# Kernel optimization log

Measured on AMD Instinct MI355X. Metric: run time of the kernel, lower is better.

The kernel has to match this reference:

```python
import jax, jax.numpy as jnp
import numpy as np

N = 8192       # num_nodes
F_IN = 128     # num_features
H = 32         # hidden_dim
C = 10         # num_classes
E = 262144     # num_edges (avg degree 32)
EPS = 1e-5     # BatchNorm1d eps


def setup_inputs() -> dict:
    key = jax.random.key(0)
    ks = jax.random.split(key, 24)
    rn = lambda k, shape, s=0.05: jax.random.normal(k, shape, jnp.float32) * s
    z = lambda n: jnp.zeros((n,), jnp.float32)
    return {
        "b": jax.random.normal(ks[0], (N, N), jnp.float32),
        "x": jax.random.normal(ks[1], (N, F_IN), jnp.float32),
        "edge_index": jax.random.randint(ks[2], (2, E), 0, N, jnp.int32),
        # GCNConv weights (stored [in,out]) + biases
        "W0": rn(ks[3], (F_IN, H)), "bc0": z(H),
        "W1": rn(ks[4], (H, H)),    "bc1": z(H),
        # BatchNorm affine params
        "g0": jnp.ones((H,), jnp.float32), "be0": z(H),
        "g1": jnp.ones((H,), jnp.float32), "be1": z(H),
        # autoencoder Linears (stored [in,out])
        "Wa0": rn(ks[5], (N, H)), "ba0": z(H),
        "Wa1": rn(ks[6], (H, H)), "ba1": z(H),
        "Wa2": rn(ks[7], (H, H)), "ba2": z(H),
        "Wa3": rn(ks[8], (H, N)), "ba3": z(N),
        # jump classifier: Linear(num_layers*H, C)
        "Wj": rn(ks[9], (2 * H, C)), "bj": z(C),
    }


def _gcn_conv(x, W, bias, src, dst):
    # PyG GCNConv: D^{-1/2}(A+I)D^{-1/2} X W + bias (src/dst already include self-loops)
    h = x @ W                                             # [N, out]
    deg = jax.ops.segment_sum(jnp.ones(src.shape[0], h.dtype), dst, num_segments=N)
    dinv = jax.lax.rsqrt(deg)                             # deg >= 1 due to self-loops
    norm = dinv[src] * dinv[dst]                          # [E+N]
    agg = jax.ops.segment_sum(norm[:, None] * h[src], dst, num_segments=N)
    return agg + bias


def _bn(x, g, b):
    # BatchNorm1d in training mode: batch stats over node dim, biased variance
    m = jnp.mean(x, axis=0)
    v = jnp.var(x, axis=0)
    return g * (x - m) * jax.lax.rsqrt(v + EPS) + b


def reference(b, x, edge_index, W0, bc0, W1, bc1, g0, be0, g1, be1,
              Wa0, ba0, Wa1, ba1, Wa2, ba2, Wa3, ba3, Wj, bj):
    loop = jnp.arange(N, dtype=edge_index.dtype)
    src = jnp.concatenate([edge_index[0], loop])
    dst = jnp.concatenate([edge_index[1], loop])

    # layer 0
    h = jax.nn.relu(_bn(_gcn_conv(x, W0, bc0, src, dst), g0, be0))
    x0 = h
    b = b @ Wa0 + ba0          # [N, H]
    h = h + b
    # layer 1
    h = jax.nn.relu(_bn(_gcn_conv(h, W1, bc1, src, dst), g1, be1))
    x1 = h
    b = b @ Wa1 + ba1
    # (torch computes x = x1 + b here, but it is dead after the last layer)
    # decoder tail: autoencoder[2], autoencoder[3]
    b = b @ Wa2 + ba2
    b = b @ Wa3 + ba3          # [N, N]

    out = jnp.concatenate([x0, x1], axis=1) @ Wj + bj
    return jax.nn.log_softmax(out, axis=-1), b
```

## Files before the change

### kernel.cpp

```cpp
#include <hip/hip_runtime.h>
#include <math.h>

#define NN 8192
#define FIN 128
#define HD 32
#define NC 10
#define NE 262144
#define EPSBN 1e-5f

typedef short short8 __attribute__((ext_vector_type(8)));
typedef float f32x4 __attribute__((ext_vector_type(4)));

__device__ __forceinline__ float bf2f(unsigned short b) {
  unsigned int u = ((unsigned int)b) << 16;
  float f;
  __builtin_memcpy(&f, &u, 4);
  return f;
}
__device__ __forceinline__ unsigned short f2bf(float f) {
  unsigned int u;
  __builtin_memcpy(&u, &f, 4);
  u = u + 0x7fffu + ((u >> 16) & 1u);
  return (unsigned short)(u >> 16);
}
__device__ __forceinline__ short8 ld_bf8(const unsigned short* p) {
  uint4 u = *(const uint4*)p;
  return __builtin_bit_cast(short8, u);
}
__device__ __forceinline__ float ldin(const void* p, int i, int isf) {
  if (isf) return ((const float*)p)[i];
  return bf2f(((const unsigned short*)p)[i]);
}

__global__ void detect_k(const void* __restrict__ b, int* __restrict__ flag) {
  const unsigned short* p = (const unsigned short*)b;
  int t = threadIdx.x;
  unsigned short s = p[2 * t];
  int e = (s >> 7) & 0xFF;
  int hit = (e >= 110 && e <= 135) ? 1 : 0;
  __shared__ int cnt[256];
  cnt[t] = hit;
  __syncthreads();
  for (int o = 128; o > 0; o >>= 1) {
    if (t < o) cnt[t] += cnt[t + o];
    __syncthreads();
  }
  if (t == 0) flag[0] = (cnt[0] < 128) ? 1 : 0;
}

__global__ void prep_T(const void* __restrict__ Wa1, const void* __restrict__ ba1,
                       const void* __restrict__ Wa2, const void* __restrict__ ba2,
                       const int* __restrict__ flg, float* __restrict__ T, float* __restrict__ vv) {
  int isf = *flg;
  __shared__ float sW1[1024], sW2[1024];
  int t = threadIdx.x;
  sW1[t] = ldin(Wa1, t, isf);
  sW2[t] = ldin(Wa2, t, isf);
  __syncthreads();
  {
    int c = t >> 5, c2 = t & 31;
    float acc = 0.f;
    for (int k = 0; k < 32; k++) acc += sW1[c * 32 + k] * sW2[k * 32 + c2];
    T[c * 32 + c2] = acc;
  }
  if (t < 32) {
    float acc = ldin(ba2, t, isf);
    for (int k = 0; k < 32; k++) acc += ldin(ba1, k, isf) * sW2[k * 32 + t];
    vv[t] = acc;
  }
}

__global__ void compute_Rp(const void* __restrict__ Wa3, const void* __restrict__ ba3,
                           const float* __restrict__ T, const float* __restrict__ vv,
                           const int* __restrict__ flg,
                           float* __restrict__ r2, unsigned short* __restrict__ Rp) {
  int isf = *flg;
  __shared__ float sT[1024], sv[32];
  int t = threadIdx.x;
  for (int i = t; i < 1024; i += 256) sT[i] = T[i];
  if (t < 32) sv[t] = vv[t];
  __syncthreads();
  int j = blockIdx.x * 256 + t;
  float w3[32];
  for (int c = 0; c < 32; c++) w3[c] = ldin(Wa3, c * NN + j, isf);
  float rr = ldin(ba3, j, isf);
  for (int c = 0; c < 32; c++) rr += sv[c] * w3[c];
  r2[j] = rr;
  float Rcol[32];
  for (int c = 0; c < 32; c++) {
    float acc = 0.f;
    for (int cp = 0; cp < 32; cp++) acc += sT[c * 32 + cp] * w3[cp];
    Rcol[c] = acc;
  }
  int jt = j >> 4, n = j & 15;
  for (int q = 0; q < 4; q++)
    for (int jj = 0; jj < 8; jj++)
      Rp[(size_t)(jt * 64 + q * 16 + n) * 8 + jj] = f2bf(Rcol[q * 8 + jj]);
}

__global__ void pack_Bp(const void* __restrict__ Wa0, const int* __restrict__ flg,
                        unsigned short* __restrict__ Bp) {
  int isf = *flg;
  int tid = blockIdx.x * 256 + threadIdx.x;
  int kb = tid >> 7;
  int h = (tid >> 6) & 1;
  int L = tid & 63;
  int q = L >> 4, n = L & 15;
  int base_k = kb * 32 + q * 8;
  if (isf) {
    const float* W = (const float*)Wa0;
    for (int j = 0; j < 8; j++)
      Bp[(size_t)((kb * 2 + h) * 64 + L) * 8 + j] = f2bf(W[(base_k + j) * HD + h * 16 + n]);
  } else {
    const unsigned short* W = (const unsigned short*)Wa0;
    for (int j = 0; j < 8; j++)
      Bp[(size_t)((kb * 2 + h) * 64 + L) * 8 + j] = W[(base_k + j) * HD + h * 16 + n];
  }
}

__global__ void deg_k(const int* __restrict__ dst, int* __restrict__ deg) {
  int e = blockIdx.x * 256 + threadIdx.x;
  atomicAdd(&deg[dst[e]], 1);
}

__global__ void csr_scan(const int* __restrict__ deg, int* __restrict__ rowp,
                         float* __restrict__ dinvf) {
  __shared__ int ps[1024];
  int t = threadIdx.x;
  int base = t * 8;
  int loc[8];
  int s = 0;
  for (int j = 0; j < 8; j++) {
    int d = deg[base + j];
    loc[j] = s;
    s += d;
    dinvf[base + j] = rsqrtf((float)d + 1.0f);
  }
  ps[t] = s;
  __syncthreads();
  for (int off = 1; off < 1024; off <<= 1) {
    int v = (t >= off) ? ps[t - off] : 0;
    __syncthreads();
    if (t >= off) ps[t] += v;
    __syncthreads();
  }
  int ex = (t > 0) ? ps[t - 1] : 0;
  for (int j = 0; j < 8; j++) rowp[base + j] = ex + loc[j];
  if (t == 1023) rowp[NN] = ex + s;
}

__global__ void csr_fill(const int* __restrict__ src, const int* __restrict__ dst,
                         const int* __restrict__ rowp, int* __restrict__ cnt,
                         int* __restrict__ col) {
  int e = blockIdx.x * 256 + threadIdx.x;
  int d = dst[e];
  int pos = atomicAdd(&cnt[d], 1);
  col[rowp[d] + pos] = src[e];
}

__global__ void gemm_x_w0(const void* __restrict__ x, const void* __restrict__ W0,
                          const float* __restrict__ dinvf, const int* __restrict__ flg,
                          float* __restrict__ h0) {
  int isf = *flg;
  __shared__ float sW[FIN * HD];
  __shared__ float sx[8 * FIN];
  int t = threadIdx.x;
  for (int i = t; i < FIN * HD; i += 256) sW[i] = ldin(W0, i, isf);
  int row0 = blockIdx.x * 8;
  for (int i = t; i < 8 * FIN; i += 256) {
    int r = i >> 7, k = i & 127;
    sx[i] = ldin(x, (row0 + r) * FIN + k, isf);
  }
  __syncthreads();
  int r = t >> 5, c = t & 31;
  float acc = 0.f;
  for (int k = 0; k < FIN; k++) acc += sx[r * FIN + k] * sW[k * HD + c];
  h0[(row0 + r) * HD + c] = acc * dinvf[row0 + r];
}

__global__ void gather_agg(const int* __restrict__ rowp, const int* __restrict__ col,
                           const float* __restrict__ dinvf, const float* __restrict__ hs,
                           float* __restrict__ agg) {
  int w = (blockIdx.x << 2) + (threadIdx.x >> 6);
  int L = threadIdx.x & 63;
  int c = L & 31, half = L >> 5;
  int s0 = rowp[w], s1 = rowp[w + 1];
  float acc = 0.f;
  int e = s0 + half;
  if (e < s1) {
    int s = col[e];
    for (e += 2; e < s1; e += 2) {
      int sn = col[e];
      acc += hs[(size_t)s * HD + c];
      s = sn;
    }
    acc += hs[(size_t)s * HD + c];
  }
  acc += __shfl_xor(acc, 32);
  if (half == 0) {
    float tot = acc + hs[(size_t)w * HD + c];
    agg[(size_t)w * HD + c] = dinvf[w] * tot;
  }
}

__global__ void bn_stats(const float* __restrict__ xin, float* __restrict__ sum, float* __restrict__ sq) {
  int t = threadIdx.x;
  int c = t & 31;
  int g = t >> 5;
  float s = 0.f, q = 0.f;
  for (int r = blockIdx.x * 8 + g; r < NN; r += 2048) {
    float v = xin[r * HD + c];
    s += v;
    q += v * v;
  }
  __shared__ float ss[256], qq[256];
  ss[t] = s; qq[t] = q;
  __syncthreads();
  if (t < 128) { ss[t] += ss[t + 128]; qq[t] += qq[t + 128]; }
  __syncthreads();
  if (t < 64) { ss[t] += ss[t + 64]; qq[t] += qq[t + 64]; }
  __syncthreads();
  if (t < 32) {
    atomicAdd(&sum[c], ss[t] + ss[t + 32]);
    atomicAdd(&sq[c], qq[t] + qq[t + 32]);
  }
}

__global__ void bn_coef(const float* __restrict__ sum, const float* __restrict__ sq,
                        const void* __restrict__ g, const void* __restrict__ be,
                        const int* __restrict__ flg, float* __restrict__ a, float* __restrict__ bb) {
  int isf = *flg;
  int c = threadIdx.x;
  if (c < 32) {
    float m = sum[c] * (1.0f / 8192.0f);
    float var = fmaxf(sq[c] * (1.0f / 8192.0f) - m * m, 0.0f);
    float rstd = rsqrtf(var + EPSBN);
    float ac = ldin(g, c, isf) * rstd;
    a[c] = ac;
    bb[c] = ldin(be, c, isf) - m * ac;
  }
}

__global__ void gemm_b_wa0(const void* __restrict__ Bm, const unsigned short* __restrict__ Bp,
                           const int* __restrict__ flg, float* __restrict__ b1) {
  int isf = *flg;
  __shared__ float red[8][512];
  int t = threadIdx.x;
  int kq = t >> 6;
  int L = t & 63;
  int rt = blockIdx.x;
  int q = L >> 4, n = L & 15;
  size_t aoff = (size_t)(rt * 16 + n) * NN + kq * 1024 + q * 8;
  f32x4 acc0 = {0.f, 0.f, 0.f, 0.f};
  f32x4 acc1 = {0.f, 0.f, 0.f, 0.f};
  int kb0 = kq * 32;
  if (isf) {
    const float* arow = (const float*)Bm + aoff;
    for (int i = 0; i < 32; i++) {
      f32x4 u0 = *(const f32x4*)(arow + i * 32);
      f32x4 u1 = *(const f32x4*)(arow + i * 32 + 4);
      union { unsigned short s[8]; short8 v; } au;
      au.s[0] = f2bf(u0[0]); au.s[1] = f2bf(u0[1]); au.s[2] = f2bf(u0[2]); au.s[3] = f2bf(u0[3]);
      au.s[4] = f2bf(u1[0]); au.s[5] = f2bf(u1[1]); au.s[6] = f2bf(u1[2]); au.s[7] = f2bf(u1[3]);
      const unsigned short* bpp = Bp + (size_t)((kb0 + i) * 2) * 512 + L * 8;
      acc0 = __builtin_amdgcn_mfma_f32_16x16x32_bf16(au.v, ld_bf8(bpp), acc0, 0, 0, 0);
      acc1 = __builtin_amdgcn_mfma_f32_16x16x32_bf16(au.v, ld_bf8(bpp + 512), acc1, 0, 0, 0);
    }
  } else {
    const unsigned short* arow = (const unsigned short*)Bm + aoff;
    for (int i = 0; i < 32; i++) {
      short8 a = ld_bf8(arow + i * 32);
      const unsigned short* bpp = Bp + (size_t)((kb0 + i) * 2) * 512 + L * 8;
      acc0 = __builtin_amdgcn_mfma_f32_16x16x32_bf16(a, ld_bf8(bpp), acc0, 0, 0, 0);
      acc1 = __builtin_amdgcn_mfma_f32_16x16x32_bf16(a, ld_bf8(bpp + 512), acc1, 0, 0, 0);
    }
  }
  for (int r = 0; r < 4; r++) {
    red[kq][(q * 4 + r) * 32 + n] = acc0[r];
    red[kq][(q * 4 + r) * 32 + n + 16] = acc1[r];
  }
  __syncthreads();
  float s = 0.f;
  for (int kw = 0; kw < 8; kw++) s += red[kw][t];
  b1[rt * 512 + t] = s;
}

__global__ void fuse0(float* __restrict__ aggA, const float* __restrict__ b1,
                      const void* __restrict__ ba0, const float* __restrict__ a,
                      const float* __restrict__ bb, const int* __restrict__ flg,
                      float* __restrict__ x0) {
  int isf = *flg;
  int i = blockIdx.x * 256 + threadIdx.x;
  int c = i & 31;
  float xv = fmaxf(a[c] * aggA[i] + bb[c], 0.0f);
  x0[i] = xv;
  aggA[i] = xv + b1[i] + ldin(ba0, c, isf);
}

__global__ void gemm_h_w1(float* __restrict__ hbuf, const void* __restrict__ W1,
                          const float* __restrict__ dinvf, const int* __restrict__ flg) {
  int isf = *flg;
  __shared__ float sW[1024], sh[256];
  int t = threadIdx.x;
  for (int i = t; i < 1024; i += 256) sW[i] = ldin(W1, i, isf);
  int row0 = blockIdx.x * 8;
  {
    int r = t >> 5, k = t & 31;
    sh[t] = hbuf[(row0 + r) * HD + k];
  }
  __syncthreads();
  int r = t >> 5, c = t & 31;
  float acc = 0.f;
  for (int k = 0; k < 32; k++) acc += sh[r * 32 + k] * sW[k * HD + c];
  hbuf[(row0 + r) * HD + c] = acc * dinvf[row0 + r];
}

__global__ void classifier(const float* __restrict__ x0, const float* __restrict__ agg1,
                           const float* __restrict__ a1, const float* __restrict__ bb1,
                           const void* __restrict__ Wj, const void* __restrict__ bj,
                           const int* __restrict__ flg, void* __restrict__ outv) {
  int isf = *flg;
  __shared__ float sW[64 * NC];
  __shared__ float sb[NC];
  __shared__ float sa[HD], sbb[HD];
  __shared__ float sx0[64 * 33], sx1[64 * 33];
  int t = threadIdx.x;
  for (int i = t; i < 64 * NC; i += 64) sW[i] = ldin(Wj, i, isf);
  if (t < NC) sb[t] = ldin(bj, t, isf);
  if (t < HD) { sa[t] = a1[t]; sbb[t] = bb1[t]; }
  int row0 = blockIdx.x * 64;
  for (int i = t; i < 64 * HD; i += 64) {
    int r = i >> 5, k = i & 31;
    sx0[r * 33 + k] = x0[(size_t)row0 * HD + i];
    sx1[r * 33 + k] = agg1[(size_t)row0 * HD + i];
  }
  __syncthreads();
  float lg[NC];
  for (int c = 0; c < NC; c++) lg[c] = sb[c];
  for (int k = 0; k < HD; k++) {
    float v = sx0[t * 33 + k];
    for (int c = 0; c < NC; c++) lg[c] += v * sW[k * NC + c];
  }
  for (int k = 0; k < HD; k++) {
    float v = fmaxf(sa[k] * sx1[t * 33 + k] + sbb[k], 0.0f);
    for (int c = 0; c < NC; c++) lg[c] += v * sW[(HD + k) * NC + c];
  }
  float mx = lg[0];
  for (int c = 1; c < NC; c++) mx = fmaxf(mx, lg[c]);
  float se = 0.f;
  for (int c = 0; c < NC; c++) se += expf(lg[c] - mx);
  float lse = mx + logf(se);
  int row = row0 + t;
  if (isf) {
    float* o = (float*)outv;
    for (int c = 0; c < NC; c++) o[row * NC + c] = lg[c] - lse;
  } else {
    unsigned short* o = (unsigned short*)outv;
    for (int c = 0; c < NC; c++) o[row * NC + c] = f2bf(lg[c] - lse);
  }
}

__global__ void gemm_b4(const float* __restrict__ b1, const void* __restrict__ ba0,
                        const unsigned short* __restrict__ Rp, const float* __restrict__ r2,
                        const int* __restrict__ flg, void* __restrict__ outv) {
  int isf = *flg;
  int t = threadIdx.x;
  int w = (blockIdx.x << 2) + (t >> 6);
  int L = t & 63;
  int rt = w >> 3, jc = w & 7;
  int q = L >> 4, n = L & 15;
  const float* ap = b1 + (size_t)(rt * 16 + n) * HD + q * 8;
  union { unsigned short s[8]; short8 v; } au;
  for (int j = 0; j < 8; j++) au.s[j] = f2bf(ap[j] + ldin(ba0, q * 8 + j, isf));
  short8 afrag = au.v;
  int orow = rt * 16 + q * 4;
  float* of = (float*)outv + NN * NC;
  unsigned short* ob = (unsigned short*)outv + NN * NC;
  for (int jt = jc * 64; jt < (jc + 1) * 64; jt++) {
    short8 bfrag = ld_bf8(Rp + (size_t)(jt * 64 + L) * 8);
    f32x4 acc = {0.f, 0.f, 0.f, 0.f};
    acc = __builtin_amdgcn_mfma_f32_16x16x32_bf16(afrag, bfrag, acc, 0, 0, 0);
    int col = jt * 16 + n;
    float radd = r2[col];
    size_t base = (size_t)orow * NN + col;
    if (isf) {
      of[base] = acc[0] + radd;
      of[base + NN] = acc[1] + radd;
      of[base + 2 * NN] = acc[2] + radd;
      of[base + 3 * NN] = acc[3] + radd;
    } else {
      ob[base] = f2bf(acc[0] + radd);
      ob[base + NN] = f2bf(acc[1] + radd);
      ob[base + 2 * NN] = f2bf(acc[2] + radd);
      ob[base + 3 * NN] = f2bf(acc[3] + radd);
    }
  }
}

extern "C" void kernel_launch(void* const* d_in, const int* in_sizes, int n_in,
                              void* d_out, int out_size, void* d_ws, size_t ws_size,
                              hipStream_t stream) {
  const void* B   = d_in[0];
  const void* X   = d_in[1];
  const int* EI   = (const int*)d_in[2];
  const void* W0  = d_in[3];
  const void* W1  = d_in[5];
  const void* g0  = d_in[7];
  const void* be0 = d_in[8];
  const void* g1  = d_in[9];
  const void* be1 = d_in[10];
  const void* Wa0 = d_in[11];
  const void* ba0 = d_in[12];
  const void* Wa1 = d_in[13];
  const void* ba1 = d_in[14];
  const void* Wa2 = d_in[15];
  const void* ba2 = d_in[16];
  const void* Wa3 = d_in[17];
  const void* ba3 = d_in[18];
  const void* Wj  = d_in[19];
  const void* bj  = d_in[20];
  (void)in_sizes; (void)n_in; (void)ws_size;

  const int* esrc = EI;
  const int* edst = EI + NE;

  float* ws   = (float*)d_ws;
  int* flag   = (int*)ws;
  float* stats = ws + 16;
  float* sum0 = stats, * sq0 = stats + 32, * sum1 = stats + 64, * sq1 = stats + 96;
  float* a0c = stats + 128, * bb0c = stats + 160, * a1c = stats + 192, * bb1c = stats + 224;
  float* b1   = stats + 256;
  float* r2   = b1 + NN * HD;
  float* T    = r2 + NN;
  float* vv   = T + 1024;
  unsigned short* Rp = (unsigned short*)(vv + 32);

  size_t outBytesMin = (size_t)out_size * 2;
  size_t scratchBytes = (size_t)(NN + 3 * NN * HD) * 4
                      + (size_t)(256 * 2 * 64 * 8) * 2
                      + (size_t)(3 * NN + 1 + NE) * 4;
  char* sc = (char*)d_out + ((outBytesMin - scratchBytes) & ~(size_t)255);
  float* degf = (float*)sc;
  float* aggA = degf + NN;
  float* aggB = aggA + NN * HD;
  float* x0h  = aggB + NN * HD;
  unsigned short* Bp = (unsigned short*)(x0h + NN * HD);
  int* deg_i  = (int*)(Bp + 256 * 2 * 64 * 8);
  int* cnt    = deg_i + NN;
  int* rowp   = cnt + NN;
  int* col    = rowp + NN + 1;

  hipMemsetAsync(ws, 0, (size_t)(16 + 256) * sizeof(float), stream);
  hipMemsetAsync(deg_i, 0, (size_t)2 * NN * sizeof(int), stream);

  detect_k<<<1, 256, 0, stream>>>(B, flag);
  prep_T<<<1, 1024, 0, stream>>>(Wa1, ba1, Wa2, ba2, flag, T, vv);
  compute_Rp<<<32, 256, 0, stream>>>(Wa3, ba3, T, vv, flag, r2, Rp);
  pack_Bp<<<128, 256, 0, stream>>>(Wa0, flag, Bp);
  deg_k<<<NE / 256, 256, 0, stream>>>(edst, deg_i);
  csr_scan<<<1, 1024, 0, stream>>>(deg_i, rowp, degf);
  csr_fill<<<NE / 256, 256, 0, stream>>>(esrc, edst, rowp, cnt, col);
  gemm_x_w0<<<NN / 8, 256, 0, stream>>>(X, W0, degf, flag, x0h);
  gemm_b_wa0<<<512, 512, 0, stream>>>(B, Bp, flag, b1);
  gather_agg<<<NN / 4, 256, 0, stream>>>(rowp, col, degf, x0h, aggA);
  bn_stats<<<256, 256, 0, stream>>>(aggA, sum0, sq0);
  bn_coef<<<1, 64, 0, stream>>>(sum0, sq0, g0, be0, flag, a0c, bb0c);
  fuse0<<<NN * HD / 256, 256, 0, stream>>>(aggA, b1, ba0, a0c, bb0c, flag, x0h);
  gemm_h_w1<<<NN / 8, 256, 0, stream>>>(aggA, W1, degf, flag);
  gather_agg<<<NN / 4, 256, 0, stream>>>(rowp, col, degf, aggA, aggB);
  bn_stats<<<256, 256, 0, stream>>>(aggB, sum1, sq1);
  bn_coef<<<1, 64, 0, stream>>>(sum1, sq1, g1, be1, flag, a1c, bb1c);
  classifier<<<NN / 64, 64, 0, stream>>>(x0h, aggB, a1c, bb1c, Wj, bj, flag, d_out);
  gemm_b4<<<1024, 256, 0, stream>>>(b1, ba0, Rp, r2, flag, d_out);
}
```

Measured before the change: 772.4 us.

## Fuse small kernels, drop memsets, and vectorize output stores in gemm_b4

```diff
diff --git a/kernel.cpp b/kernel.cpp
--- a/kernel.cpp
+++ b/kernel.cpp
@@ -10,6 +10,7 @@
 
 typedef short short8 __attribute__((ext_vector_type(8)));
 typedef float f32x4 __attribute__((ext_vector_type(4)));
+typedef unsigned short us4 __attribute__((ext_vector_type(4)));
 
 __device__ __forceinline__ float bf2f(unsigned short b) {
   unsigned int u = ((unsigned int)b) << 16;
@@ -32,7 +33,8 @@
   return bf2f(((const unsigned short*)p)[i]);
 }
 
-__global__ void detect_k(const void* __restrict__ b, int* __restrict__ flag) {
+__global__ void detect_k(const void* __restrict__ b, int* __restrict__ flag,
+                         float* __restrict__ stats, int* __restrict__ dz) {
   const unsigned short* p = (const unsigned short*)b;
   int t = threadIdx.x;
   unsigned short s = p[2 * t];
@@ -40,6 +42,8 @@
   int hit = (e >= 110 && e <= 135) ? 1 : 0;
   __shared__ int cnt[256];
   cnt[t] = hit;
+  stats[t] = 0.0f;
+  for (int i = t; i < 2 * NN; i += 256) dz[i] = 0;
   __syncthreads();
   for (int o = 128; o > 0; o >>= 1) {
     if (t < o) cnt[t] += cnt[t + o];
@@ -48,37 +52,30 @@
   if (t == 0) flag[0] = (cnt[0] < 128) ? 1 : 0;
 }
 
-__global__ void prep_T(const void* __restrict__ Wa1, const void* __restrict__ ba1,
-                       const void* __restrict__ Wa2, const void* __restrict__ ba2,
-                       const int* __restrict__ flg, float* __restrict__ T, float* __restrict__ vv) {
-  int isf = *flg;
-  __shared__ float sW1[1024], sW2[1024];
-  int t = threadIdx.x;
-  sW1[t] = ldin(Wa1, t, isf);
-  sW2[t] = ldin(Wa2, t, isf);
-  __syncthreads();
-  {
-    int c = t >> 5, c2 = t & 31;
+__global__ void compute_Rp(const void* __restrict__ Wa1, const void* __restrict__ ba1,
+                           const void* __restrict__ Wa2, const void* __restrict__ ba2,
+                           const void* __restrict__ Wa3, const void* __restrict__ ba3,
+                           const int* __restrict__ flg,
+                           float* __restrict__ r2, unsigned short* __restrict__ Rp) {
+  int isf = *flg;
+  __shared__ float sW1[1024], sW2[1024], sT[1024], sv[32];
+  int t = threadIdx.x;
+  for (int i = t; i < 1024; i += 256) {
+    sW1[i] = ldin(Wa1, i, isf);
+    sW2[i] = ldin(Wa2, i, isf);
+  }
+  __syncthreads();
+  for (int i = t; i < 1024; i += 256) {
+    int c = i >> 5, c2 = i & 31;
     float acc = 0.f;
     for (int k = 0; k < 32; k++) acc += sW1[c * 32 + k] * sW2[k * 32 + c2];
-    T[c * 32 + c2] = acc;
+    sT[i] = acc;
   }
   if (t < 32) {
     float acc = ldin(ba2, t, isf);
     for (int k = 0; k < 32; k++) acc += ldin(ba1, k, isf) * sW2[k * 32 + t];
-    vv[t] = acc;
-  }
-}
-
-__global__ void compute_Rp(const void* __restrict__ Wa3, const void* __restrict__ ba3,
-                           const float* __restrict__ T, const float* __restrict__ vv,
-                           const int* __restrict__ flg,
-                           float* __restrict__ r2, unsigned short* __restrict__ Rp) {
-  int isf = *flg;
-  __shared__ float sT[1024], sv[32];
-  int t = threadIdx.x;
-  for (int i = t; i < 1024; i += 256) sT[i] = T[i];
-  if (t < 32) sv[t] = vv[t];
+    sv[t] = acc;
+  }
   __syncthreads();
   int j = blockIdx.x * 256 + t;
   float w3[32];
@@ -226,19 +223,30 @@
   }
 }
 
-__global__ void bn_coef(const float* __restrict__ sum, const float* __restrict__ sq,
-                        const void* __restrict__ g, const void* __restrict__ be,
-                        const int* __restrict__ flg, float* __restrict__ a, float* __restrict__ bb) {
-  int isf = *flg;
-  int c = threadIdx.x;
-  if (c < 32) {
-    float m = sum[c] * (1.0f / 8192.0f);
-    float var = fmaxf(sq[c] * (1.0f / 8192.0f) - m * m, 0.0f);
-    float rstd = rsqrtf(var + EPSBN);
-    float ac = ldin(g, c, isf) * rstd;
-    a[c] = ac;
-    bb[c] = ldin(be, c, isf) - m * ac;
-  }
+__global__ void fuse0_w1(float* __restrict__ aggA, const float* __restrict__ b1,
+                         const void* __restrict__ ba0, const void* __restrict__ W1,
+                         const float* __restrict__ sum0, const float* __restrict__ sq0,
+                         const void* __restrict__ g0, const void* __restrict__ be0,
+                         const float* __restrict__ dinvf, const int* __restrict__ flg,
+                         float* __restrict__ x0) {
+  int isf = *flg;
+  __shared__ float sW[1024], sh[16 * 33];
+  int t = threadIdx.x;
+  for (int i = t; i < 1024; i += 512) sW[i] = ldin(W1, i, isf);
+  int r = t >> 5, c = t & 31;
+  int row = blockIdx.x * 16 + r;
+  float m = sum0[c] * (1.0f / 8192.0f);
+  float var = fmaxf(sq0[c] * (1.0f / 8192.0f) - m * m, 0.0f);
+  float ac = ldin(g0, c, isf) * rsqrtf(var + EPSBN);
+  float bc = ldin(be0, c, isf) - m * ac;
+  float v = aggA[row * HD + c];
+  float xv = fmaxf(ac * v + bc, 0.0f);
+  x0[row * HD + c] = xv;
+  sh[r * 33 + c] = xv + b1[row * HD + c] + ldin(ba0, c, isf);
+  __syncthreads();
+  float acc = 0.f;
+  for (int k = 0; k < 32; k++) acc += sh[r * 33 + k] * sW[k * HD + c];
+  aggA[row * HD + c] = acc * dinvf[row];
 }
 
 __global__ void gemm_b_wa0(const void* __restrict__ Bm, const unsigned short* __restrict__ Bp,
@@ -285,38 +293,9 @@
   b1[rt * 512 + t] = s;
 }
 
-__global__ void fuse0(float* __restrict__ aggA, const float* __restrict__ b1,
-                      const void* __restrict__ ba0, const float* __restrict__ a,
-                      const float* __restrict__ bb, const int* __restrict__ flg,
-                      float* __restrict__ x0) {
-  int isf = *flg;
-  int i = blockIdx.x * 256 + threadIdx.x;
-  int c = i & 31;
-  float xv = fmaxf(a[c] * aggA[i] + bb[c], 0.0f);
-  x0[i] = xv;
-  aggA[i] = xv + b1[i] + ldin(ba0, c, isf);
-}
-
-__global__ void gemm_h_w1(float* __restrict__ hbuf, const void* __restrict__ W1,
-                          const float* __restrict__ dinvf, const int* __restrict__ flg) {
-  int isf = *flg;
-  __shared__ float sW[1024], sh[256];
-  int t = threadIdx.x;
-  for (int i = t; i < 1024; i += 256) sW[i] = ldin(W1, i, isf);
-  int row0 = blockIdx.x * 8;
-  {
-    int r = t >> 5, k = t & 31;
-    sh[t] = hbuf[(row0 + r) * HD + k];
-  }
-  __syncthreads();
-  int r = t >> 5, c = t & 31;
-  float acc = 0.f;
-  for (int k = 0; k < 32; k++) acc += sh[r * 32 + k] * sW[k * HD + c];
-  hbuf[(row0 + r) * HD + c] = acc * dinvf[row0 + r];
-}
-
 __global__ void classifier(const float* __restrict__ x0, const float* __restrict__ agg1,
-                           const float* __restrict__ a1, const float* __restrict__ bb1,
+                           const float* __restrict__ sum1, const float* __restrict__ sq1,
+                           const void* __restrict__ g1, const void* __restrict__ be1,
                            const void* __restrict__ Wj, const void* __restrict__ bj,
                            const int* __restrict__ flg, void* __restrict__ outv) {
   int isf = *flg;
@@ -327,7 +306,13 @@
   int t = threadIdx.x;
   for (int i = t; i < 64 * NC; i += 64) sW[i] = ldin(Wj, i, isf);
   if (t < NC) sb[t] = ldin(bj, t, isf);
-  if (t < HD) { sa[t] = a1[t]; sbb[t] = bb1[t]; }
+  if (t < HD) {
+    float m = sum1[t] * (1.0f / 8192.0f);
+    float var = fmaxf(sq1[t] * (1.0f / 8192.0f) - m * m, 0.0f);
+    float ac = ldin(g1, t, isf) * rsqrtf(var + EPSBN);
+    sa[t] = ac;
+    sbb[t] = ldin(be1, t, isf) - m * ac;
+  }
   int row0 = blockIdx.x * 64;
   for (int i = t; i < 64 * HD; i += 64) {
     int r = i >> 5, k = i & 31;
@@ -372,27 +357,24 @@
   const float* ap = b1 + (size_t)(rt * 16 + n) * HD + q * 8;
   union { unsigned short s[8]; short8 v; } au;
   for (int j = 0; j < 8; j++) au.s[j] = f2bf(ap[j] + ldin(ba0, q * 8 + j, isf));
-  short8 afrag = au.v;
-  int orow = rt * 16 + q * 4;
+  short8 bfrag = au.v;
+  int orow = rt * 16 + n;
   float* of = (float*)outv + NN * NC;
   unsigned short* ob = (unsigned short*)outv + NN * NC;
   for (int jt = jc * 64; jt < (jc + 1) * 64; jt++) {
-    short8 bfrag = ld_bf8(Rp + (size_t)(jt * 64 + L) * 8);
+    short8 afrag = ld_bf8(Rp + (size_t)(jt * 64 + L) * 8);
     f32x4 acc = {0.f, 0.f, 0.f, 0.f};
     acc = __builtin_amdgcn_mfma_f32_16x16x32_bf16(afrag, bfrag, acc, 0, 0, 0);
-    int col = jt * 16 + n;
-    float radd = r2[col];
+    int col = jt * 16 + q * 4;
+    f32x4 radd = *(const f32x4*)(r2 + col);
+    f32x4 res = acc + radd;
     size_t base = (size_t)orow * NN + col;
     if (isf) {
-      of[base] = acc[0] + radd;
-      of[base + NN] = acc[1] + radd;
-      of[base + 2 * NN] = acc[2] + radd;
-      of[base + 3 * NN] = acc[3] + radd;
+      *(f32x4*)(of + base) = res;
     } else {
-      ob[base] = f2bf(acc[0] + radd);
-      ob[base + NN] = f2bf(acc[1] + radd);
-      ob[base + 2 * NN] = f2bf(acc[2] + radd);
-      ob[base + 3 * NN] = f2bf(acc[3] + radd);
+      us4 pk;
+      pk[0] = f2bf(res[0]); pk[1] = f2bf(res[1]); pk[2] = f2bf(res[2]); pk[3] = f2bf(res[3]);
+      *(us4*)(ob + base) = pk;
     }
   }
 }
@@ -428,12 +410,9 @@
   int* flag   = (int*)ws;
   float* stats = ws + 16;
   float* sum0 = stats, * sq0 = stats + 32, * sum1 = stats + 64, * sq1 = stats + 96;
-  float* a0c = stats + 128, * bb0c = stats + 160, * a1c = stats + 192, * bb1c = stats + 224;
   float* b1   = stats + 256;
   float* r2   = b1 + NN * HD;
-  float* T    = r2 + NN;
-  float* vv   = T + 1024;
-  unsigned short* Rp = (unsigned short*)(vv + 32);
+  unsigned short* Rp = (unsigned short*)(r2 + NN);
 
   size_t outBytesMin = (size_t)out_size * 2;
   size_t scratchBytes = (size_t)(NN + 3 * NN * HD) * 4
@@ -450,12 +429,8 @@
   int* rowp   = cnt + NN;
   int* col    = rowp + NN + 1;
 
-  hipMemsetAsync(ws, 0, (size_t)(16 + 256) * sizeof(float), stream);
-  hipMemsetAsync(deg_i, 0, (size_t)2 * NN * sizeof(int), stream);
-
-  detect_k<<<1, 256, 0, stream>>>(B, flag);
-  prep_T<<<1, 1024, 0, stream>>>(Wa1, ba1, Wa2, ba2, flag, T, vv);
-  compute_Rp<<<32, 256, 0, stream>>>(Wa3, ba3, T, vv, flag, r2, Rp);
+  detect_k<<<1, 256, 0, stream>>>(B, flag, stats, deg_i);
+  compute_Rp<<<32, 256, 0, stream>>>(Wa1, ba1, Wa2, ba2, Wa3, ba3, flag, r2, Rp);
   pack_Bp<<<128, 256, 0, stream>>>(Wa0, flag, Bp);
   deg_k<<<NE / 256, 256, 0, stream>>>(edst, deg_i);
   csr_scan<<<1, 1024, 0, stream>>>(deg_i, rowp, degf);
@@ -464,12 +439,10 @@
   gemm_b_wa0<<<512, 512, 0, stream>>>(B, Bp, flag, b1);
   gather_agg<<<NN / 4, 256, 0, stream>>>(rowp, col, degf, x0h, aggA);
   bn_stats<<<256, 256, 0, stream>>>(aggA, sum0, sq0);
-  bn_coef<<<1, 64, 0, stream>>>(sum0, sq0, g0, be0, flag, a0c, bb0c);
-  fuse0<<<NN * HD / 256, 256, 0, stream>>>(aggA, b1, ba0, a0c, bb0c, flag, x0h);
-  gemm_h_w1<<<NN / 8, 256, 0, stream>>>(aggA, W1, degf, flag);
+  fuse0_w1<<<NN / 16, 512, 0, stream>>>(aggA, b1, ba0, W1, sum0, sq0, g0, be0,
+                                        degf, flag, x0h);
   gather_agg<<<NN / 4, 256, 0, stream>>>(rowp, col, degf, aggA, aggB);
   bn_stats<<<256, 256, 0, stream>>>(aggB, sum1, sq1);
-  bn_coef<<<1, 64, 0, stream>>>(sum1, sq1, g1, be1, flag, a1c, bb1c);
-  classifier<<<NN / 64, 64, 0, stream>>>(x0h, aggB, a1c, bb1c, Wj, bj, flag, d_out);
+  classifier<<<NN / 64, 64, 0, stream>>>(x0h, aggB, sum1, sq1, g1, be1, Wj, bj, flag, d_out);
   gemm_b4<<<1024, 256, 0, stream>>>(b1, ba0, Rp, r2, flag, d_out);
 }
```

Result: faster. 748.0 us (-3.2%).
